# Kernel optimization log

Hardware: AMD Instinct MI355X
Metric: run time of the kernel (lower is better)

Reference implementation:

```python
import jax, jax.numpy as jnp
from jax import lax
import numpy as np

B, T, IN, H, L, C = 1024, 64, 64, 512, 8, 128


def setup_inputs() -> dict:
    key = jax.random.key(0)
    ks = jax.random.split(key, 11)
    s_in = 1.0 / np.sqrt(H)
    return {
        "x": jax.random.normal(ks[0], (B, T, IN), jnp.float32),
        "w_ih0": jax.random.normal(ks[1], (4 * H, IN), jnp.float32) * s_in,
        "w_hh0": jax.random.normal(ks[2], (4 * H, H), jnp.float32) * s_in,
        "b_ih0": jax.random.normal(ks[3], (4 * H,), jnp.float32) * s_in,
        "b_hh0": jax.random.normal(ks[4], (4 * H,), jnp.float32) * s_in,
        "w_ih": jax.random.normal(ks[5], (L - 1, 4 * H, H), jnp.float32) * s_in,
        "w_hh": jax.random.normal(ks[6], (L - 1, 4 * H, H), jnp.float32) * s_in,
        "b_ih": jax.random.normal(ks[7], (L - 1, 4 * H), jnp.float32) * s_in,
        "b_hh": jax.random.normal(ks[8], (L - 1, 4 * H), jnp.float32) * s_in,
        "fc_w": jax.random.normal(ks[9], (C, H * T), jnp.float32) * (1.0 / np.sqrt(H * T)),
        "fc_b": jax.random.normal(ks[10], (C,), jnp.float32) * 0.01,
    }


def _lstm_layer(x_tbd, wi, wh, bi, bh):
    # x_tbd: [T, B, D_in]; returns hidden sequence [T, B, H]
    b = x_tbd.shape[1]
    h_dim = wh.shape[1]
    bias = bi + bh

    def step(carry, x_t):
        h, c = carry
        gates = x_t @ wi.T + h @ wh.T + bias  # [B, 4H]
        i, f, g, o = jnp.split(gates, 4, axis=-1)  # PyTorch gate order i,f,g,o
        i = jax.nn.sigmoid(i)
        f = jax.nn.sigmoid(f)
        g = jnp.tanh(g)
        o = jax.nn.sigmoid(o)
        c = f * c + i * g
        h = o * jnp.tanh(c)
        return (h, c), h

    h0 = jnp.zeros((b, h_dim), x_tbd.dtype)
    _, hs = lax.scan(step, (h0, h0), x_tbd)
    return hs


def reference(x, w_ih0, w_hh0, b_ih0, b_hh0, w_ih, w_hh, b_ih, b_hh, fc_w, fc_b):
    xt = jnp.transpose(x, (1, 0, 2))  # [T, B, IN]
    h = _lstm_layer(xt, w_ih0, w_hh0, b_ih0, b_hh0)
    for l in range(w_ih.shape[0]):  # fixed small layer count
        h = _lstm_layer(h, w_ih[l], w_hh[l], b_ih[l], b_hh[l])
    out = jnp.transpose(h, (1, 0, 2)).reshape(x.shape[0], -1)  # [B, T*H]
    return out @ fc_w.T + fc_b
```

## Files before the change

kernel.cpp:

```cpp
#include <hip/hip_runtime.h>
#include <hip/hip_bf16.h>

#define BB   1024
#define TT   64
#define IND  64
#define HH   512
#define G4   2048
#define NLAYER 8
#define NCLS 128
#define KP   1024
#define RS   8
#define SLOT (32 * 1024 * 16)

typedef __bf16 bf16x8 __attribute__((ext_vector_type(8)));
typedef float  f32x4  __attribute__((ext_vector_type(4)));

typedef const __attribute__((address_space(1))) void* as1cvp;
typedef __attribute__((address_space(3))) void* as3vp;

__device__ __forceinline__ void gload16(void* lds, const void* g) {
  __builtin_amdgcn_global_load_lds((as1cvp)g, (as3vp)lds, 16, 0, 0);
}

__device__ __forceinline__ float sigmf(float x) { return 1.f / (1.f + __expf(-x)); }
__device__ __forceinline__ float tanhfast(float x) { return 2.f / (1.f + __expf(-2.f * x)) - 1.f; }

__global__ void cvt_kernel(const float* __restrict__ s, __bf16* __restrict__ d, int n) {
  int i = blockIdx.x * 256 + threadIdx.x;
  if (i < n) d[i] = (__bf16)s[i];
}

__global__ void pack_w(const float* __restrict__ whh0, const float* __restrict__ wih0,
                       const float* __restrict__ whh, const float* __restrict__ wih,
                       __bf16* __restrict__ Wp) {
  int i = blockIdx.x * 256 + threadIdx.x;
  int k = i & (KP - 1), n = (i >> 10) & 2047, l = i >> 21;
  float v;
  if (k < 512) v = (l == 0) ? whh0[n * 512 + k] : whh[((size_t)(l - 1) * G4 + n) * 512 + k];
  else if (l == 0) v = (k < 512 + IND) ? wih0[n * IND + (k - 512)] : 0.f;
  else v = wih[((size_t)(l - 1) * G4 + n) * 512 + (k - 512)];
  Wp[i] = (__bf16)v;
}

__global__ void bias_prep(const float* __restrict__ bi0, const float* __restrict__ bh0,
                          const float* __restrict__ bi, const float* __restrict__ bh,
                          float* __restrict__ biasb) {
  int i = blockIdx.x * 256 + threadIdx.x;
  int l = i >> 11, k = i & 2047;
  float v = (l == 0) ? (bi0[k] + bh0[k]) : (bi[(l - 1) * G4 + k] + bh[(l - 1) * G4 + k]);
  biasb[i] = v;
}

__global__ void zero_u32(unsigned* __restrict__ p, int n) {
  int i = blockIdx.x * 256 + threadIdx.x;
  if (i < n) p[i] = 0u;
}

__global__ __launch_bounds__(256, 2) void lstm_all(
    const float* __restrict__ xf,
    const __bf16* __restrict__ Wp,
    const float* __restrict__ biasb,
    __bf16* __restrict__ hring,
    __bf16* __restrict__ h7,
    unsigned* __restrict__ flags,
    unsigned* __restrict__ xslot) {
  extern __shared__ __bf16 Wlds[];
  __shared__ int sbs;
  const int tid = threadIdx.x;

  if (tid == 0) {
    unsigned xcc;
    asm volatile("s_getreg_b32 %0, hwreg(HW_REG_XCC_ID)" : "=s"(xcc));
    xcc &= 7u;
    unsigned slot = __hip_atomic_fetch_add(xslot + xcc, 1u, __ATOMIC_RELAXED,
                                           __HIP_MEMORY_SCOPE_AGENT) & 63u;
    sbs = (int)((xcc << 6) | slot);
  }
  __syncthreads();
  const int l  = sbs >> 6;
  const int bx = (sbs >> 5) & 1;
  const int by = sbs & 31;
  const int j0 = by << 4;
  const __bf16* Wl = Wp + (size_t)l * G4 * KP;

  for (int it = 0; it < 16; ++it) {
    const int p = it * 256 + tid;
    const int kt = p >> 8;
    const int q = p & 255;
    const int u = q >> 2;
    const int g = (q & 3) ^ ((u >> 1) & 3);
    const int n = ((u >> 4) << 9) + j0 + (u & 15);
    gload16(&Wlds[p * 8], Wl + (size_t)n * KP + kt * 32 + g * 8);
  }

  const int lane = tid & 63, wv = tid >> 6;
  const int qr = lane >> 4, ml = lane & 15;
  const __bf16* wb[4];
  float bv[4];
  int wsw[4];
#pragma unroll
  for (int g = 0; g < 4; ++g) {
    const int n = g * 512 + j0 + ml;
    wb[g] = Wl + (size_t)n * KP + 512 + qr * 8;
    bv[g] = biasb[l * G4 + n];
    const int u = g * 16 + ml;
    wsw[g] = u * 32 + ((qr ^ ((u >> 1) & 3)) << 3);
  }
  const int r0 = (bx << 9) + (wv << 7);
  const int rowA = r0 + ml;
  const int abase = ((qr >> 1) << 14) + rowA * 16 + ((qr & 1) << 3);
  __bf16* ringL = hring + (size_t)l * RS * SLOT;
  const __bf16* ringU = hring + (size_t)((l > 0 ? l : 1) - 1) * RS * SLOT;
  unsigned* ownfw = flags + ((l * 2 + bx) * 4 + wv) * 32;
  unsigned* upfw  = flags + (((l > 0 ? l - 1 : 0) * 2 + bx) * 4 + wv) * 32;
  unsigned* dnfw  = flags + (((l < 7 ? l + 1 : 7) * 2 + bx) * 4 + wv) * 32;
  float c8[8][4] = {};
  f32x4 acc[8][4];
  __syncthreads();

  auto pollge = [&](const unsigned* fp, unsigned need) {
    for (;;) {
      unsigned v = (lane < 32) ? __hip_atomic_load(fp + lane, __ATOMIC_RELAXED,
                                                   __HIP_MEMORY_SCOPE_AGENT)
                               : need;
      if (__all((int)(v >= need))) break;
      __builtin_amdgcn_s_sleep(1);
    }
    asm volatile("" ::: "memory");
    __builtin_amdgcn_sched_barrier(0);
  };

  auto initAcc = [&]() {
#pragma unroll
    for (int m = 0; m < 8; ++m)
#pragma unroll
      for (int g = 0; g < 4; ++g)
#pragma unroll
        for (int r = 0; r < 4; ++r) acc[m][g][r] = bv[g];
  };

  auto xpartL0 = [&](int tx) {
#pragma unroll
    for (int m = 0; m < 8; ++m) {
      const float* xr = xf + ((size_t)(rowA + m * 16) * TT + tx) * IND + qr * 8;
      const f32x4 f0 = *(const f32x4*)xr;
      const f32x4 f1 = *(const f32x4*)(xr + 4);
      const f32x4 f2 = *(const f32x4*)(xr + 32);
      const f32x4 f3 = *(const f32x4*)(xr + 36);
      bf16x8 a0, a1;
#pragma unroll
      for (int r = 0; r < 4; ++r) {
        a0[r] = (__bf16)f0[r]; a0[4 + r] = (__bf16)f1[r];
        a1[r] = (__bf16)f2[r]; a1[4 + r] = (__bf16)f3[r];
      }
#pragma unroll
      for (int g = 0; g < 4; ++g) {
        acc[m][g] = __builtin_amdgcn_mfma_f32_16x16x32_bf16(
            a0, *(const bf16x8*)(wb[g]), acc[m][g], 0, 0, 0);
        acc[m][g] = __builtin_amdgcn_mfma_f32_16x16x32_bf16(
            a1, *(const bf16x8*)(wb[g] + 32), acc[m][g], 0, 0, 0);
      }
    }
  };

  auto xpartL = [&](int tx) {
    const __bf16* src = ringU + (size_t)(tx & (RS - 1)) * SLOT + abase;
    bf16x8 A0[4], A1[4], Wr[2][4];
#pragma unroll
    for (int m = 0; m < 4; ++m) A0[m] = *(const bf16x8*)(src + m * 256);
#pragma unroll
    for (int m = 0; m < 4; ++m) A1[m] = *(const bf16x8*)(src + (4 + m) * 256);
#pragma unroll
    for (int g = 0; g < 4; ++g) Wr[0][g] = *(const bf16x8*)(wb[g]);
#pragma unroll
    for (int kt = 0; kt < 16; ++kt) {
      const __bf16* aknx = src + (kt + 1) * 32768;
#pragma unroll
      for (int m = 0; m < 4; ++m)
#pragma unroll
        for (int g = 0; g < 4; ++g)
          acc[m][g] = __builtin_amdgcn_mfma_f32_16x16x32_bf16(
              A0[m], Wr[kt & 1][g], acc[m][g], 0, 0, 0);
      if (kt < 15) {
#pragma unroll
        for (int m = 0; m < 4; ++m) A0[m] = *(const bf16x8*)(aknx + m * 256);
#pragma unroll
        for (int g = 0; g < 4; ++g)
          Wr[(kt + 1) & 1][g] = *(const bf16x8*)(wb[g] + (kt + 1) * 32);
      }
      __builtin_amdgcn_sched_barrier(0);
#pragma unroll
      for (int m = 0; m < 4; ++m)
#pragma unroll
        for (int g = 0; g < 4; ++g)
          acc[4 + m][g] = __builtin_amdgcn_mfma_f32_16x16x32_bf16(
              A1[m], Wr[kt & 1][g], acc[4 + m][g], 0, 0, 0);
      if (kt < 15) {
#pragma unroll
        for (int m = 0; m < 4; ++m) A1[m] = *(const bf16x8*)(aknx + (4 + m) * 256);
      }
      __builtin_amdgcn_sched_barrier(0);
    }
  };

  auto hpart = [&](int t) {
    const __bf16* srcH = ((l < 7) ? ringL + (size_t)((t - 1) & (RS - 1)) * SLOT
                                  : h7 + (size_t)(t - 1) * SLOT) + abase;
    bf16x8 A0[4], A1[4];
#pragma unroll
    for (int m = 0; m < 4; ++m) A0[m] = *(const bf16x8*)(srcH + m * 256);
#pragma unroll
    for (int m = 0; m < 4; ++m) A1[m] = *(const bf16x8*)(srcH + (4 + m) * 256);
#pragma unroll
    for (int kt = 0; kt < 16; ++kt) {
      const __bf16* aknx = srcH + (kt + 1) * 32768;
      bf16x8 wf[4];
#pragma unroll
      for (int g = 0; g < 4; ++g) wf[g] = *(const bf16x8*)&Wlds[kt * 2048 + wsw[g]];
#pragma unroll
      for (int m = 0; m < 4; ++m)
#pragma unroll
        for (int g = 0; g < 4; ++g)
          acc[m][g] = __builtin_amdgcn_mfma_f32_16x16x32_bf16(
              A0[m], wf[g], acc[m][g], 0, 0, 0);
      if (kt < 15) {
#pragma unroll
        for (int m = 0; m < 4; ++m) A0[m] = *(const bf16x8*)(aknx + m * 256);
      }
      __builtin_amdgcn_sched_barrier(0);
#pragma unroll
      for (int m = 0; m < 4; ++m)
#pragma unroll
        for (int g = 0; g < 4; ++g)
          acc[4 + m][g] = __builtin_amdgcn_mfma_f32_16x16x32_bf16(
              A1[m], wf[g], acc[4 + m][g], 0, 0, 0);
      if (kt < 15) {
#pragma unroll
        for (int m = 0; m < 4; ++m) A1[m] = *(const bf16x8*)(aknx + (4 + m) * 256);
      }
      __builtin_amdgcn_sched_barrier(0);
    }
  };

  if (l > 0) pollge(upfw, 1u);
  initAcc();
  if (l == 0) xpartL0(0); else xpartL(0);

  for (int t = 0; t < TT; ++t) {
    if (t > 0) {
      pollge(ownfw, (unsigned)t);
      if ((t & (RS - 1)) == 0)
        __builtin_amdgcn_fence(__ATOMIC_ACQUIRE, "agent");
      hpart(t);
    }

    if (l < 7 && t >= RS) pollge(dnfw, (unsigned)(t - (RS - 1)));

    unsigned short* dst = (unsigned short*)(((l < 7)
        ? ringL + (size_t)(t & (RS - 1)) * SLOT
        : h7 + (size_t)t * SLOT) + ((size_t)by << 14)) + ml;
#pragma unroll
    for (int m = 0; m < 8; ++m) {
      const int rbm = r0 + m * 16 + (qr << 2);
#pragma unroll
      for (int r = 0; r < 4; ++r) {
        const float gi = sigmf(acc[m][0][r]);
        const float gf = sigmf(acc[m][1][r]);
        const float gg = tanhfast(acc[m][2][r]);
        const float go = sigmf(acc[m][3][r]);
        const float cv = gf * c8[m][r] + gi * gg;
        c8[m][r] = cv;
        const __bf16 hv = (__bf16)(go * tanhfast(cv));
        __hip_atomic_store(dst + (size_t)(rbm + r) * 16,
                           __builtin_bit_cast(unsigned short, hv),
                           __ATOMIC_RELAXED, __HIP_MEMORY_SCOPE_AGENT);
      }
    }
    asm volatile("s_waitcnt vmcnt(0)" ::: "memory");
    __builtin_amdgcn_sched_barrier(0);
    if (lane == 0)
      __hip_atomic_store(ownfw + by, (unsigned)(t + 1), __ATOMIC_RELAXED,
                         __HIP_MEMORY_SCOPE_AGENT);

    if (t + 1 < TT) {
      if (l > 0) pollge(upfw, (unsigned)(t + 2));
      initAcc();
      if (l == 0) xpartL0(t + 1); else xpartL(t + 1);
    }
  }
}

__global__ __launch_bounds__(256, 2) void fc_kernel(
    const __bf16* __restrict__ hseq, const __bf16* __restrict__ fcw,
    float* __restrict__ partial) {
  __shared__ __bf16 At[64 * 32];
  __shared__ __bf16 Wt[128 * 32];
  const int tid = threadIdx.x;
  const int b0 = blockIdx.x * 64;
  const int kbase = blockIdx.y * 2048;
  const int lane = tid & 63, wv = tid >> 6;
  const int qr = lane >> 4, ml = lane & 15;
  const int wr = (wv >> 1) * 32, wc = (wv & 1) * 64;
  const int sr = tid >> 2, sk = (tid & 3) * 8;

  f32x4 acc[2][4];
  for (int i = 0; i < 2; i++)
    for (int j = 0; j < 4; j++)
      for (int r = 0; r < 4; r++) acc[i][j][r] = 0.f;

  for (int kt = 0; kt < 64; ++kt) {
    const int k = kbase + kt * 32;
    const int t = k >> 9;
    const int kk = (k & 511) + sk;
    gload16(&At[tid * 8],
            hseq + (size_t)t * SLOT + ((size_t)(kk >> 4) * 1024 + b0 + sr) * 16 + (kk & 15));
    gload16(&Wt[tid * 8],        fcw + (size_t)sr * (TT * HH) + k + sk);
    gload16(&Wt[2048 + tid * 8], fcw + (size_t)(sr + 64) * (TT * HH) + k + sk);
    __syncthreads();
    bf16x8 af[2], bfr[4];
    for (int i = 0; i < 2; i++) af[i]  = *(const bf16x8*)&At[(wr + i * 16 + ml) * 32 + qr * 8];
    for (int j = 0; j < 4; j++) bfr[j] = *(const bf16x8*)&Wt[(wc + j * 16 + ml) * 32 + qr * 8];
    for (int i = 0; i < 2; i++)
      for (int j = 0; j < 4; j++)
        acc[i][j] = __builtin_amdgcn_mfma_f32_16x16x32_bf16(af[i], bfr[j], acc[i][j], 0, 0, 0);
    __syncthreads();
  }
  for (int i = 0; i < 2; i++)
    for (int j = 0; j < 4; j++)
      for (int r = 0; r < 4; r++)
        partial[((size_t)blockIdx.y * BB + b0 + wr + i * 16 + qr * 4 + r) * NCLS + wc + j * 16 + ml] =
            acc[i][j][r];
}

__global__ void fc_reduce(const float* __restrict__ partial, const float* __restrict__ fcb,
                          float* __restrict__ out) {
  int i = blockIdx.x * 256 + threadIdx.x;
  float s = fcb[i & 127];
  for (int p = 0; p < 16; p++) s += partial[(size_t)p * (BB * NCLS) + i];
  out[i] = s;
}

extern "C" void kernel_launch(void* const* d_in, const int* in_sizes, int n_in,
                              void* d_out, int out_size, void* d_ws, size_t ws_size,
                              hipStream_t stream) {
  const float* x    = (const float*)d_in[0];
  const float* wih0 = (const float*)d_in[1];
  const float* whh0 = (const float*)d_in[2];
  const float* bih0 = (const float*)d_in[3];
  const float* bhh0 = (const float*)d_in[4];
  const float* wih  = (const float*)d_in[5];
  const float* whh  = (const float*)d_in[6];
  const float* bih  = (const float*)d_in[7];
  const float* bhh  = (const float*)d_in[8];
  const float* fcw  = (const float*)d_in[9];
  const float* fcb  = (const float*)d_in[10];
  float* out = (float*)d_out;

  hipFuncSetAttribute((const void*)lstm_all,
                      hipFuncAttributeMaxDynamicSharedMemorySize, 65536);

  size_t off = 0;
  char* base = (char*)d_ws;
  auto carve = [&](size_t bytes) -> char* {
    char* p = base + off;
    off += (bytes + 255) & ~(size_t)255;
    return p;
  };
  __bf16*   Wp    = (__bf16*)carve((size_t)NLAYER * G4 * KP * 2);
  __bf16*   fcwb  = (__bf16*)carve((size_t)NCLS * TT * HH * 2);
  float*    biasb = (float*)carve((size_t)NLAYER * G4 * 4);
  __bf16*   hring = (__bf16*)carve((size_t)7 * RS * SLOT * 2);
  __bf16*   h7    = (__bf16*)carve((size_t)TT * SLOT * 2);
  float*    part  = (float*)carve((size_t)16 * BB * NCLS * 4);
  unsigned* flags = (unsigned*)carve((size_t)(NLAYER * 2 * 4 * 32 + 64) * 4);
  unsigned* xslot = flags + NLAYER * 2 * 4 * 32;

  pack_w<<<(NLAYER * G4 * KP) / 256, 256, 0, stream>>>(whh0, wih0, whh, wih, Wp);
  cvt_kernel<<<(NCLS * TT * HH) / 256, 256, 0, stream>>>(fcw, fcwb, NCLS * TT * HH);
  bias_prep<<<(NLAYER * G4) / 256, 256, 0, stream>>>(bih0, bhh0, bih, bhh, biasb);
  zero_u32<<<(NLAYER * 2 * 4 * 32 + 64 + 255) / 256, 256, 0, stream>>>(
      flags, NLAYER * 2 * 4 * 32 + 64);

  lstm_all<<<512, 256, 65536, stream>>>(x, Wp, biasb, hring, h7, flags, xslot);

  fc_kernel<<<dim3(16, 16), 256, 0, stream>>>(h7, fcwb, part);
  fc_reduce<<<(BB * NCLS) / 256, 256, 0, stream>>>(part, fcb, out);
}
```

Before: 3.687 ms.

## Consume recurrent and input h slices incrementally as producer flags arrive

Replaces the blocking wait on all 32 producer flags before each recurrent and input-projection GEMM with a single check. If every flag is ready, the original pipelined path runs. Otherwise a fallback walks the 16 K-tiles, polls only the two flags covering each tile, then issues its MFMAs. This lets compute start on the parts of h that are already written instead of stalling on the slowest producer. In exchange the fallback path loses software prefetch pipelining and adds a poll per tile.

```diff
diff --git a/kernel.cpp b/kernel.cpp
--- a/kernel.cpp
+++ b/kernel.cpp
@@ -129,6 +129,26 @@
     asm volatile("" ::: "memory");
     __builtin_amdgcn_sched_barrier(0);
   };
+  auto allge = [&](const unsigned* fp, unsigned need) -> bool {
+    unsigned v = (lane < 32) ? __hip_atomic_load(fp + lane, __ATOMIC_RELAXED,
+                                                 __HIP_MEMORY_SCOPE_AGENT)
+                             : need;
+    const bool ok = __all((int)(v >= need));
+    asm volatile("" ::: "memory");
+    __builtin_amdgcn_sched_barrier(0);
+    return ok;
+  };
+  auto poll2 = [&](const unsigned* fp, int p, unsigned need) {
+    for (;;) {
+      unsigned v = (lane < 2) ? __hip_atomic_load(fp + 2 * p + lane, __ATOMIC_RELAXED,
+                                                  __HIP_MEMORY_SCOPE_AGENT)
+                              : need;
+      if (__all((int)(v >= need))) break;
+      __builtin_amdgcn_s_sleep(1);
+    }
+    asm volatile("" ::: "memory");
+    __builtin_amdgcn_sched_barrier(0);
+  };
 
   auto initAcc = [&]() {
 #pragma unroll
@@ -203,6 +223,27 @@
     }
   };
 
+  auto xpartLInc = [&](int tx) {
+    const __bf16* src = ringU + (size_t)(tx & (RS - 1)) * SLOT + abase;
+    const unsigned need = (unsigned)(tx + 1);
+#pragma unroll 1
+    for (int kt = 0; kt < 16; ++kt) {
+      poll2(upfw, kt, need);
+      const __bf16* ak = src + kt * 32768;
+      bf16x8 wf[4];
+#pragma unroll
+      for (int g = 0; g < 4; ++g) wf[g] = *(const bf16x8*)(wb[g] + kt * 32);
+      bf16x8 A[8];
+#pragma unroll
+      for (int m = 0; m < 8; ++m) A[m] = *(const bf16x8*)(ak + m * 256);
+#pragma unroll
+      for (int m = 0; m < 8; ++m)
+#pragma unroll
+        for (int g = 0; g < 4; ++g)
+          acc[m][g] = __builtin_amdgcn_mfma_f32_16x16x32_bf16(A[m], wf[g], acc[m][g], 0, 0, 0);
+    }
+  };
+
   auto hpart = [&](int t) {
     const __bf16* srcH = ((l < 7) ? ringL + (size_t)((t - 1) & (RS - 1)) * SLOT
                                   : h7 + (size_t)(t - 1) * SLOT) + abase;
@@ -242,16 +283,41 @@
     }
   };
 
-  if (l > 0) pollge(upfw, 1u);
+  auto hpartInc = [&](int t) {
+    const __bf16* srcH = ((l < 7) ? ringL + (size_t)((t - 1) & (RS - 1)) * SLOT
+                                  : h7 + (size_t)(t - 1) * SLOT) + abase;
+    const unsigned need = (unsigned)t;
+#pragma unroll 1
+    for (int kt = 0; kt < 16; ++kt) {
+      poll2(ownfw, kt, need);
+      const __bf16* ak = srcH + kt * 32768;
+      bf16x8 wf[4];
+#pragma unroll
+      for (int g = 0; g < 4; ++g) wf[g] = *(const bf16x8*)&Wlds[kt * 2048 + wsw[g]];
+      bf16x8 A[8];
+#pragma unroll
+      for (int m = 0; m < 8; ++m) A[m] = *(const bf16x8*)(ak + m * 256);
+#pragma unroll
+      for (int m = 0; m < 8; ++m)
+#pragma unroll
+        for (int g = 0; g < 4; ++g)
+          acc[m][g] = __builtin_amdgcn_mfma_f32_16x16x32_bf16(A[m], wf[g], acc[m][g], 0, 0, 0);
+    }
+  };
+
   initAcc();
-  if (l == 0) xpartL0(0); else xpartL(0);
+  if (l == 0) {
+    xpartL0(0);
+  } else {
+    if (allge(upfw, 1u)) xpartL(0); else xpartLInc(0);
+  }
 
   for (int t = 0; t < TT; ++t) {
     if (t > 0) {
-      pollge(ownfw, (unsigned)t);
+      const bool ok = allge(ownfw, (unsigned)t);
       if ((t & (RS - 1)) == 0)
         __builtin_amdgcn_fence(__ATOMIC_ACQUIRE, "agent");
-      hpart(t);
+      if (ok) hpart(t); else hpartInc(t);
     }
 
     if (l < 7 && t >= RS) pollge(dnfw, (unsigned)(t - (RS - 1)));
@@ -283,9 +349,12 @@
                          __HIP_MEMORY_SCOPE_AGENT);
 
     if (t + 1 < TT) {
-      if (l > 0) pollge(upfw, (unsigned)(t + 2));
       initAcc();
-      if (l == 0) xpartL0(t + 1); else xpartL(t + 1);
+      if (l == 0) {
+        xpartL0(t + 1);
+      } else {
+        if (allge(upfw, (unsigned)(t + 2))) xpartL(t + 1); else xpartLInc(t + 1);
+      }
     }
   }
 }
```

New measurement: 5.544 ms. 1.5x slower.
